# Optimization experiments

Hardware: AMD Instinct MI355X
Metric: run time of the kernel (lower is better)

Reference implementation:

```python
import jax, jax.numpy as jnp
import numpy as np

EPS = 1e-5
NUM_GROUPS = 32
NUM_HEADS = 4


def setup_inputs() -> dict:
    key = jax.random.key(0)
    k1, k2, k3 = jax.random.split(key, 3)
    b, c, h, w = 8, 256, 32, 32
    x = jax.random.normal(k1, (b, c, h, w), dtype=jnp.float32)
    gn_w = jnp.ones((c,), dtype=jnp.float32)
    gn_b = jnp.zeros((c,), dtype=jnp.float32)
    qkv_w = jax.random.normal(k2, (3 * c, c), dtype=jnp.float32) * (1.0 / np.sqrt(c))
    qkv_b = jnp.zeros((3 * c,), dtype=jnp.float32)
    proj_w = jax.random.normal(k3, (c, c), dtype=jnp.float32) * (1.0 / np.sqrt(c))
    proj_b = jnp.zeros((c,), dtype=jnp.float32)
    return {"x": x, "gn_w": gn_w, "gn_b": gn_b, "qkv_w": qkv_w,
            "qkv_b": qkv_b, "proj_w": proj_w, "proj_b": proj_b}


def _group_norm(x, weight, bias):
    # x: (b, c, n)
    b, c, n = x.shape
    xg = x.reshape(b, NUM_GROUPS, (c // NUM_GROUPS) * n)
    mean = jnp.mean(xg, axis=-1, keepdims=True)
    var = jnp.mean(jnp.square(xg - mean), axis=-1, keepdims=True)
    xn = ((xg - mean) * jax.lax.rsqrt(var + EPS)).reshape(b, c, n)
    return xn * weight[None, :, None] + bias[None, :, None]


def reference(x, gn_w, gn_b, qkv_w, qkv_b, proj_w, proj_b):
    b, c, h, w = x.shape
    # FFT2 over spatial dims, then view_as_real -> flatten: seq len N = 2*h*w
    xf = jnp.fft.fft2(x)                                   # (b,c,h,w) complex64
    xr = jnp.stack([xf.real, xf.imag], axis=-1).reshape(b, c, -1)  # (b,c,N)
    n = xr.shape[-1]
    # GroupNorm(32, c) then 1x1 Conv1d producing qkv
    normed = _group_norm(xr, gn_w, gn_b)
    qkv = jnp.einsum('oc,bcn->bon', qkv_w, normed) + qkv_b[None, :, None]  # (b,3c,N)
    # split heads exactly like torch: view(b*H, 3c/H, N) then split along dim 1
    qkv = qkv.reshape(b * NUM_HEADS, 3 * c // NUM_HEADS, n)
    ch = c // NUM_HEADS
    q, k, v = qkv[:, :ch], qkv[:, ch:2 * ch], qkv[:, 2 * ch:]
    scale = ch ** -0.25
    weight = jnp.einsum('bct,bcs->bts', q * scale, k * scale)  # (b*H, N, N)
    weight = jax.nn.softmax(weight, axis=-1)
    a = jnp.einsum('bts,bcs->bct', weight, v).reshape(b, c, n)
    out = jnp.einsum('oc,bcn->bon', proj_w, a) + proj_b[None, :, None]  # (b,c,N)
    # back to complex and IFFT2
    out = out.reshape(b, c, h, w, 2)
    oc = jax.lax.complex(out[..., 0], out[..., 1])
    res = jnp.fft.ifft2(oc)                                # (b,c,h,w) complex64
    # return complex result as real/imag pair
    return jnp.stack([res.real, res.imag], axis=-1)         # (b,c,h,w,2)
```

## Files before the change

kernel.cpp:

```cpp
#include <hip/hip_runtime.h>
#include <hip/hip_bf16.h>

#define PI_F 3.14159265358979323846f
#define C1_EXP 0.18033688f
#define C2_EXP 23.083120f

typedef __bf16 bf16x8 __attribute__((ext_vector_type(8)));
typedef float f32x4 __attribute__((ext_vector_type(4)));
typedef unsigned int uint32x4 __attribute__((ext_vector_type(4)));

__device__ __forceinline__ bf16x8 neg8(bf16x8 v) {
  union { bf16x8 b; uint32x4 u; } x;
  x.b = v;
  x.u ^= (uint32x4){0x80008000u, 0x80008000u, 0x80008000u, 0x80008000u};
  return x.b;
}

#define MFMA3(acc, Ph, Pl, Qh, Ql)                                        \
  acc = __builtin_amdgcn_mfma_f32_16x16x32_bf16(Ph, Qh, acc, 0, 0, 0);    \
  acc = __builtin_amdgcn_mfma_f32_16x16x32_bf16(Ph, Ql, acc, 0, 0, 0);    \
  acc = __builtin_amdgcn_mfma_f32_16x16x32_bf16(Pl, Qh, acc, 0, 0, 0);

__device__ __forceinline__ int slot2n(int slot) {
  const int pi = slot >> 1, im = slot & 1;
  int k1, k2;
  if (pi < 480)      { k1 = 1 + (pi >> 5); k2 = pi & 31; }
  else if (pi < 495) { k1 = 0;  k2 = pi - 479; }
  else if (pi < 510) { k1 = 16; k2 = pi - 494; }
  else if (pi < 514) { k1 = ((pi - 510) >> 1) * 16; k2 = ((pi - 510) & 1) * 16; }
  else               { k1 = 0; k2 = 0; }
  return 2 * (k1 * 32 + k2) + im;
}

__global__ __launch_bounds__(256) void k_twid(__bf16* __restrict__ tw) {
  for (int e = threadIdx.x; e < 1024; e += 256) {
    const int j = e >> 5, k = e & 31;
    const int t = (j * k) & 31;
    float sv, cv;
    sincosf(2.0f * PI_F * (float)t / 32.0f, &sv, &cv);
    const __bf16 ch = (__bf16)cv;
    const __bf16 sh = (__bf16)sv;
    tw[e] = ch;
    tw[1024 + e] = (__bf16)(cv - (float)ch);
    tw[2048 + e] = sh;
    tw[3072 + e] = (__bf16)(sv - (float)sh);
  }
}

__global__ __launch_bounds__(256) void k_fft2(const float* __restrict__ x,
                                              float* __restrict__ xr,
                                              float* __restrict__ stats_raw,
                                              const __bf16* __restrict__ tw) {
  __shared__ __align__(16) char smem[51200];
  const int tid = threadIdx.x, lane = tid & 63, wv = tid >> 6;
  const int quad = lane >> 4, q16 = lane & 15;
  const int slice = blockIdx.x * 4 + wv;
  char* const wr_ = smem + 10240 + wv * 10240;

  const float* xs = x + (size_t)slice * 1024;
  float4 xv[4];
#pragma unroll
  for (int u = 0; u < 4; ++u) xv[u] = ((const float4*)xs)[u * 64 + lane];

  for (int i = tid; i < 512; i += 256) {
    const int t = i >> 7, r = (i >> 2) & 31, c8 = (i & 3) * 8;
    *(uint4*)(smem + t * 2560 + r * 80 + c8 * 2) =
        *(const uint4*)(tw + t * 1024 + r * 32 + c8);
  }

#pragma unroll
  for (int u = 0; u < 4; ++u) {
    const int f = u * 64 + lane;
    const float4 v = xv[u];
    const int row = f >> 3, c4 = (f & 7) * 4;
    union { unsigned long long q; __bf16 b[4]; } ph, pl;
    ph.b[0] = (__bf16)v.x; ph.b[1] = (__bf16)v.y;
    ph.b[2] = (__bf16)v.z; ph.b[3] = (__bf16)v.w;
    pl.b[0] = (__bf16)(v.x - (float)ph.b[0]);
    pl.b[1] = (__bf16)(v.y - (float)ph.b[1]);
    pl.b[2] = (__bf16)(v.z - (float)ph.b[2]);
    pl.b[3] = (__bf16)(v.w - (float)ph.b[3]);
    *(unsigned long long*)(wr_ + row * 80 + c4 * 2) = ph.q;
    *(unsigned long long*)(wr_ + 2560 + row * 80 + c4 * 2) = pl.q;
  }
  __syncthreads();

  bf16x8 cch[2], ccl[2], ssh[2], ssl[2], xh[2], xl[2];
#pragma unroll
  for (int t2 = 0; t2 < 2; ++t2) {
    const int row = t2 * 16 + q16;
    cch[t2] = *(const bf16x8*)(smem + row * 80 + quad * 16);
    ccl[t2] = *(const bf16x8*)(smem + 2560 + row * 80 + quad * 16);
    ssh[t2] = *(const bf16x8*)(smem + 5120 + row * 80 + quad * 16);
    ssl[t2] = *(const bf16x8*)(smem + 7680 + row * 80 + quad * 16);
    xh[t2] = *(const bf16x8*)(wr_ + row * 80 + quad * 16);
    xl[t2] = *(const bf16x8*)(wr_ + 2560 + row * 80 + quad * 16);
  }

  f32x4 yre[2][2] = {}, yim[2][2] = {};
#pragma unroll
  for (int mt = 0; mt < 2; ++mt)
#pragma unroll
    for (int nt = 0; nt < 2; ++nt) {
      MFMA3(yre[mt][nt], xh[mt], xl[mt], cch[nt], ccl[nt]);
      MFMA3(yim[mt][nt], xh[mt], xl[mt], ssh[nt], ssl[nt]);
    }

#pragma unroll
  for (int mt = 0; mt < 2; ++mt)
#pragma unroll
    for (int nt = 0; nt < 2; ++nt) {
      char* base = wr_ + (nt * 16 + q16) * 80 + (mt * 16 + quad * 4) * 2;
      union { unsigned long long q; __bf16 b[4]; } h, l;
#pragma unroll
      for (int r = 0; r < 4; ++r) {
        const float v = yre[mt][nt][r];
        h.b[r] = (__bf16)v; l.b[r] = (__bf16)(v - (float)h.b[r]);
      }
      *(unsigned long long*)(base) = h.q;
      *(unsigned long long*)(base + 2560) = l.q;
#pragma unroll
      for (int r = 0; r < 4; ++r) {
        const float v = -yim[mt][nt][r];
        h.b[r] = (__bf16)v; l.b[r] = (__bf16)(v - (float)h.b[r]);
      }
      *(unsigned long long*)(base + 5120) = h.q;
      *(unsigned long long*)(base + 7680) = l.q;
    }
  asm volatile("" ::: "memory");

  bf16x8 yreh[2], yrel[2], yimh[2], yiml[2];
#pragma unroll
  for (int nt = 0; nt < 2; ++nt) {
    const int row = nt * 16 + q16;
    yreh[nt] = *(const bf16x8*)(wr_ + row * 80 + quad * 16);
    yrel[nt] = *(const bf16x8*)(wr_ + 2560 + row * 80 + quad * 16);
    yimh[nt] = *(const bf16x8*)(wr_ + 5120 + row * 80 + quad * 16);
    yiml[nt] = *(const bf16x8*)(wr_ + 7680 + row * 80 + quad * 16);
  }

  f32x4 zre[2][2] = {}, zim[2][2] = {};
  bf16x8 ssnh[2], ssnl[2];
  ssnh[0] = neg8(ssh[0]); ssnh[1] = neg8(ssh[1]);
  ssnl[0] = neg8(ssl[0]); ssnl[1] = neg8(ssl[1]);
#pragma unroll
  for (int mt = 0; mt < 2; ++mt)
#pragma unroll
    for (int nt = 0; nt < 2; ++nt) {
      MFMA3(zre[mt][nt], cch[mt], ccl[mt], yreh[nt], yrel[nt]);
      MFMA3(zre[mt][nt], ssh[mt], ssl[mt], yimh[nt], yiml[nt]);
      MFMA3(zim[mt][nt], cch[mt], ccl[mt], yimh[nt], yiml[nt]);
      MFMA3(zim[mt][nt], ssnh[mt], ssnl[mt], yreh[nt], yrel[nt]);
    }

  float* op = xr + (size_t)slice * 2048;
  float s1 = 0.f, s2 = 0.f;
#pragma unroll
  for (int mt = 0; mt < 2; ++mt)
#pragma unroll
    for (int nt = 0; nt < 2; ++nt)
#pragma unroll
      for (int r = 0; r < 4; ++r) {
        const int k1 = mt * 16 + quad * 4 + r;
        const int k2 = nt * 16 + q16;
        const float a = zre[mt][nt][r], bimg = zim[mt][nt][r];
        s1 += a + bimg;
        s2 += a * a + bimg * bimg;
        float2 st; st.x = a; st.y = bimg;
        *(float2*)(op + 2 * (k1 * 32 + k2)) = st;
      }
#pragma unroll
  for (int off = 1; off <= 32; off <<= 1) {
    s1 += __shfl_xor(s1, off);
    s2 += __shfl_xor(s2, off);
  }
  if (lane == 0) {
    const int bg = (slice >> 8) * 32 + ((slice & 255) >> 3);
    atomicAdd(&stats_raw[bg * 2], s1);
    atomicAdd(&stats_raw[bg * 2 + 1], s2);
  }
}

__global__ __launch_bounds__(256) void k_uvec(const float* __restrict__ stats_raw,
                                              const float* __restrict__ gn_w,
                                              const float* __restrict__ gn_b,
                                              const float* __restrict__ qkv_w,
                                              const float* __restrict__ qkv_b,
                                              float* __restrict__ uk,
                                              float* __restrict__ uv) {
  const int blk = blockIdx.x;
  const int tid = threadIdx.x;
  const int b = blk >> 3, h = (blk >> 1) & 3, role = blk & 1;
  __shared__ float Bsh[256];
  {
    const int g = tid >> 3;
    const float S = stats_raw[(b * 32 + g) * 2];
    const float S2 = stats_raw[(b * 32 + g) * 2 + 1];
    const float mean = S * (1.0f / 16384.0f);
    const float var = S2 * (1.0f / 16384.0f) - mean * mean;
    const float rstd = rsqrtf(var + 1e-5f);
    Bsh[tid] = gn_b[tid] - mean * rstd * gn_w[tid];
  }
  __syncthreads();
  const int cp = tid >> 2, seg = tid & 3;
  const int row = h * 192 + 64 + role * 64 + cp;
  const float* wr_ = qkv_w + (size_t)row * 256 + seg * 64;
  const float* bs = Bsh + seg * 64;
  float s = 0.f;
#pragma unroll
  for (int i = 0; i < 16; ++i) {
    const float4 w4 = *(const float4*)(wr_ + i * 4);
    const float4 b4 = *(const float4*)(bs + i * 4);
    s += w4.x * b4.x + w4.y * b4.y + w4.z * b4.z + w4.w * b4.w;
  }
  s += __shfl_xor(s, 1);
  s += __shfl_xor(s, 2);
  if (seg == 0) {
    float* dst = (role == 0) ? uk : uv;
    dst[(size_t)(b * 4 + h) * 64 + cp] = s + qkv_b[row];
  }
}

__global__ __launch_bounds__(256) void k_gntrans(const float* __restrict__ xr,
                                                 const float* __restrict__ stats_raw,
                                                 const float* __restrict__ w,
                                                 const float* __restrict__ bias,
                                                 __bf16* __restrict__ xt) {
  const int n0 = blockIdx.x * 64;
  const int c0 = blockIdx.y * 64;
  const int b = blockIdx.z;
  __shared__ __bf16 Lt[64][72];
  const int tid = threadIdx.x;
  for (int i = tid; i < 1024; i += 256) {
    const int cl = i >> 4, c = c0 + cl, nl = (i & 15) * 4;
    const float S = stats_raw[(b * 32 + (c >> 3)) * 2];
    const float S2 = stats_raw[(b * 32 + (c >> 3)) * 2 + 1];
    const float mean = S * (1.0f / 16384.0f);
    const float var = S2 * (1.0f / 16384.0f) - mean * mean;
    const float rstd = rsqrtf(var + 1e-5f);
    const float sc = rstd * w[c];
    const float sh = bias[c] - mean * sc;
    const float4 v = *(const float4*)(xr + ((size_t)b * 256 + c) * 2048 + n0 + nl);
    Lt[nl][cl] = (__bf16)(v.x * sc + sh);
    Lt[nl + 1][cl] = (__bf16)(v.y * sc + sh);
    Lt[nl + 2][cl] = (__bf16)(v.z * sc + sh);
    Lt[nl + 3][cl] = (__bf16)(v.w * sc + sh);
  }
  __syncthreads();
  __bf16* dst = xt + (size_t)b * 524288 + (size_t)n0 * 256 + c0;
  for (int i = tid; i < 512; i += 256) {
    const int nl = i >> 3, cch = (i & 7) * 8;
    *(uint4*)(dst + (size_t)nl * 256 + cch) = *(const uint4*)&Lt[nl][cch];
  }
}

__global__ __launch_bounds__(256) void k_gemm_qkv(const float* __restrict__ W,
                                                  const __bf16* __restrict__ X,
                                                  const float* __restrict__ bias,
                                                  const float* __restrict__ uk,
                                                  float* __restrict__ dq,
                                                  __bf16* __restrict__ Qt,
                                                  __bf16* __restrict__ Kt,
                                                  __bf16* __restrict__ Vt) {
  const int tx = blockIdx.x;
  const int b = blockIdx.y;
  int role, hd, nt;
  if (tx < 64) { role = 0; hd = tx >> 4; nt = tx & 15; }
  else if (tx < 100) { role = 1; const int i = tx - 64; hd = i / 9; nt = i - hd * 9; }
  else { role = 2; const int i = tx - 100; hd = i / 9; nt = i - hd * 9; }
  const int n0 = nt * 128;
  const int bo = hd * 192 + role * 64;
  const __bf16* Xb = X + (size_t)b * 524288;

  __shared__ __align__(16) char smem[30720];
  __bf16 (*Ot)[72] = (__bf16(*)[72])smem;
  __bf16 (*Ot2)[136] = (__bf16(*)[136])smem;

  const int tid = threadIdx.x, lane = tid & 63, wv = tid >> 6;
  const int quad = lane >> 4, q16 = lane & 15, wn = wv * 32;

  const int rowA = tid >> 2, chA = (tid & 3) * 8;
  const int browB0 = tid >> 2, bchB = (tid & 3) * 8;
  const float* wA = W + (size_t)(bo + rowA) * 256 + chA;

  const int s0r = n0 + browB0, s1r = n0 + browB0 + 64;
  const int pn0 = (role == 0) ? s0r : slot2n(s0r);
  const int pn1 = (role == 0) ? s1r : slot2n(s1r);

  float4 aP0 = *(const float4*)(wA);
  float4 aP1 = *(const float4*)(wA + 4);
  uint4 bP0 = *(const uint4*)(Xb + (size_t)pn0 * 256 + bchB);
  uint4 bP1 = *(const uint4*)(Xb + (size_t)pn1 * 256 + bchB);

  f32x4 acc[4][2] = {};
  int bsel = 0;
  for (int k0 = 0; k0 < 256; k0 += 32) {
    char* const Ab = smem + bsel;
    char* const Bb = smem + bsel + 5120;
    {
      union { uint4 u; __bf16 h[8]; } pa;
      pa.h[0] = (__bf16)aP0.x; pa.h[1] = (__bf16)aP0.y;
      pa.h[2] = (__bf16)aP0.z; pa.h[3] = (__bf16)aP0.w;
      pa.h[4] = (__bf16)aP1.x; pa.h[5] = (__bf16)aP1.y;
      pa.h[6] = (__bf16)aP1.z; pa.h[7] = (__bf16)aP1.w;
      *(uint4*)(Ab + rowA * 80 + chA * 2) = pa.u;
      *(uint4*)(Bb + browB0 * 80 + bchB * 2) = bP0;
      *(uint4*)(Bb + (browB0 + 64) * 80 + bchB * 2) = bP1;
    }
    __syncthreads();
    if (k0 + 32 < 256) {
      const int kn = k0 + 32;
      aP0 = *(const float4*)(wA + kn);
      aP1 = *(const float4*)(wA + kn + 4);
      bP0 = *(const uint4*)(Xb + (size_t)pn0 * 256 + kn + bchB);
      bP1 = *(const uint4*)(Xb + (size_t)pn1 * 256 + kn + bchB);
    }
    bf16x8 af[4], bfr[2];
#pragma unroll
    for (int mt = 0; mt < 4; ++mt)
      af[mt] = *(const bf16x8*)(Ab + (mt * 16 + q16) * 80 + quad * 16);
#pragma unroll
    for (int jn = 0; jn < 2; ++jn)
      bfr[jn] = *(const bf16x8*)(Bb + (wn + jn * 16 + q16) * 80 + quad * 16);
#pragma unroll
    for (int mt = 0; mt < 4; ++mt)
#pragma unroll
      for (int jn = 0; jn < 2; ++jn)
        acc[mt][jn] = __builtin_amdgcn_mfma_f32_16x16x32_bf16(af[mt], bfr[jn], acc[mt][jn], 0, 0, 0);
    bsel ^= 15360;
  }
  __syncthreads();

  const int bh = b * 4 + hd;
  if (role == 2) {
#pragma unroll
    for (int mt = 0; mt < 4; ++mt)
#pragma unroll
      for (int r = 0; r < 4; ++r) {
        const int c = mt * 16 + quad * 4 + r;
        const float bv = bias[bo + c];
#pragma unroll
        for (int jn = 0; jn < 2; ++jn)
          Ot2[c][wn + jn * 16 + q16] = (__bf16)(acc[mt][jn][r] + bv);
      }
    __syncthreads();
    __bf16* dst = Vt + (size_t)bh * 73728;
    for (int i = tid; i < 1024; i += 256) {
      const int c = i >> 4, sg = (i & 15) * 8;
      *(uint4*)(dst + (size_t)c * 1152 + n0 + sg) = *(const uint4*)&Ot2[c][sg];
    }
  } else {
    __bf16* dst = (role == 0 ? Qt + (size_t)bh * 131072
                             : Kt + (size_t)bh * 73728);
#pragma unroll
    for (int mt = 0; mt < 4; ++mt)
#pragma unroll
      for (int r = 0; r < 4; ++r) {
        const int c = mt * 16 + quad * 4 + r;
        const float bv = bias[bo + c];
#pragma unroll
        for (int jn = 0; jn < 2; ++jn)
          Ot[wn + jn * 16 + q16][c] = (__bf16)(acc[mt][jn][r] + bv);
      }
    __syncthreads();
    for (int i = tid; i < 1024; i += 256) {
      const int nl = i >> 3, cch = (i & 7) * 8;
      *(uint4*)(dst + (size_t)(n0 + nl) * 64 + cch) = *(const uint4*)&Ot[nl][cch];
    }
    if (role == 0 && tid < 128) {
      const float* ukp = uk + (size_t)bh * 64;
      float dv = 0.f;
#pragma unroll
      for (int g8 = 0; g8 < 8; ++g8) {
        const bf16x8 qv = *(const bf16x8*)&Ot[tid][g8 * 8];
#pragma unroll
        for (int k = 0; k < 8; ++k) dv += (float)qv[k] * ukp[g8 * 8 + k];
      }
      dq[(size_t)bh * 2048 + n0 + tid] = dv * (2.0f * C1_EXP);
    }
  }
}

template <bool EDGE>
__device__ __forceinline__ void attn_iter(
    const int s0, const int send, const int quad,
    const __bf16* __restrict__ kg, const __bf16* __restrict__ vg,
    char* const kw, char* const vw,
    const char* const (&krp)[2][2], const char* const (&vrp)[4],
    char* const (&pwp)[2][2], const char* const (&prp)[2],
    const bf16x8 (&bq)[2][2], const float (&Dm)[2],
    uint4& kA, uint4& vA, f32x4 (&oacc)[2][4],
    float (&lsum)[2], float (&spsum)[2]) {
  *(uint4*)kw = kA;
  *(uint4*)vw = vA;
  __syncthreads();
  if (s0 + 32 < send) {
    kA = *(const uint4*)(kg + (size_t)(s0 + 32) * 64);
    vA = *(const uint4*)(vg + s0 + 32);
  }

  f32x4 sacc[2][2] = {};
#pragma unroll
  for (int j = 0; j < 2; ++j)
#pragma unroll
    for (int kk = 0; kk < 2; ++kk) {
      const bf16x8 ak = *(const bf16x8*)krp[j][kk];
      sacc[0][j] = __builtin_amdgcn_mfma_f32_16x16x32_bf16(ak, bq[0][kk], sacc[0][j], 0, 0, 0);
      sacc[1][j] = __builtin_amdgcn_mfma_f32_16x16x32_bf16(ak, bq[1][kk], sacc[1][j], 0, 0, 0);
    }

#pragma unroll
  for (int b = 0; b < 2; ++b) {
    float lacc = 0.f, spacc = 0.f;
#pragma unroll
    for (int j = 0; j < 2; ++j) {
      float B0, B2, Bv1, Bv3, Bm1, Bm3;
      if (EDGE) {
        const int sg = s0 + j * 16 + quad * 4;
        B0 = (sg < 1020) ? (1.0f - C2_EXP) : ((sg < 1028) ? -C2_EXP : -1e30f);
        B2 = (sg + 2 < 1020) ? (1.0f - C2_EXP)
                             : ((sg + 2 < 1028) ? -C2_EXP : -1e30f);
        Bv1 = (sg + 1 < 1028) ? -C2_EXP : -1e30f;
        Bv3 = (sg + 3 < 1028) ? -C2_EXP : -1e30f;
        Bm1 = (sg + 1 < 1020) ? Dm[b] : -1e30f;
        Bm3 = (sg + 3 < 1020) ? Dm[b] : -1e30f;
      } else {
        B0 = 1.0f - C2_EXP;
        B2 = 1.0f - C2_EXP;
        Bv1 = -C2_EXP;
        Bv3 = -C2_EXP;
        Bm1 = Dm[b];
        Bm3 = Dm[b];
      }
      const float P0  = __builtin_amdgcn_exp2f(fmaf(sacc[b][j][0],  C1_EXP, B0));
      const float Pv1 = __builtin_amdgcn_exp2f(fmaf(sacc[b][j][1],  C1_EXP, Bv1));
      const float P2  = __builtin_amdgcn_exp2f(fmaf(sacc[b][j][2],  C1_EXP, B2));
      const float Pv3 = __builtin_amdgcn_exp2f(fmaf(sacc[b][j][3],  C1_EXP, Bv3));
      const float pm1 = __builtin_amdgcn_exp2f(fmaf(sacc[b][j][1], -C1_EXP, Bm1));
      const float pm3 = __builtin_amdgcn_exp2f(fmaf(sacc[b][j][3], -C1_EXP, Bm3));
      const float mm = pm1 + pm3;
      lacc += (P0 + P2) + (Pv1 + Pv3) + mm;
      spacc += mm;
      union { uint2 u; __bf16 h[4]; } pk;
      pk.h[0] = (__bf16)P0;
      pk.h[1] = (__bf16)(Pv1 - pm1);
      pk.h[2] = (__bf16)P2;
      pk.h[3] = (__bf16)(Pv3 - pm3);
      *(uint2*)pwp[b][j] = pk.u;
    }
    lsum[b] += lacc;
    spsum[b] += spacc;
  }
  asm volatile("" ::: "memory");

  bf16x8 bp[2];
  bp[0] = *(const bf16x8*)prp[0];
  bp[1] = *(const bf16x8*)prp[1];
#pragma unroll
  for (int jc = 0; jc < 4; ++jc) {
    const bf16x8 av = *(const bf16x8*)vrp[jc];
    oacc[0][jc] = __builtin_amdgcn_mfma_f32_16x16x32_bf16(av, bp[0], oacc[0][jc], 0, 0, 0);
    oacc[1][jc] = __builtin_amdgcn_mfma_f32_16x16x32_bf16(av, bp[1], oacc[1][jc], 0, 0, 0);
  }
  __syncthreads();
}

__global__ __launch_bounds__(256, 4) void k_attn_mfma(const __bf16* __restrict__ Qt,
                                                      const __bf16* __restrict__ Kt,
                                                      const __bf16* __restrict__ Vt,
                                                      const float* __restrict__ dq,
                                                      const float* __restrict__ uv,
                                                      __bf16* __restrict__ opart,
                                                      float* __restrict__ lpart) {
  const int t0 = blockIdx.x * 128;
  const int part = blockIdx.y;
  const int bh = blockIdx.z;
  const __bf16* kt = Kt + (size_t)bh * 73728;
  const __bf16* vt = Vt + (size_t)bh * 73728;

  __shared__ __align__(16) char smem[16384];

  const int tid = threadIdx.x, lane = tid & 63, wv = tid >> 6;
  const int quad = lane >> 4, q16 = lane & 15;
  const int wband = wv * 32;

  const int rK = tid >> 3, gK = tid & 7;
  char* const kw = smem + rK * 128 + ((gK ^ (rK & 7)) * 16);
  const int cV = tid >> 2, gV = tid & 3;
  char* const vw = smem + 4096 + (cV >> 1) * 128 +
                   ((((cV & 1) * 4 + gV) ^ ((cV >> 1) & 7)) * 16);
  const __bf16* const kg = kt + (size_t)rK * 64 + gK * 8;
  const __bf16* const vg = vt + (size_t)cV * 1152 + gV * 8;

  const char* krp[2][2];
#pragma unroll
  for (int j = 0; j < 2; ++j)
#pragma unroll
    for (int kk = 0; kk < 2; ++kk)
      krp[j][kk] = smem + (j * 16 + q16) * 128 + (((kk * 4 + quad) ^ (q16 & 7)) * 16);
  const int a7 = (q16 >> 1) & 7, p1 = q16 & 1;
  const char* vrp[4];
#pragma unroll
  for (int jc = 0; jc < 4; ++jc)
    vrp[jc] = smem + 4096 + (jc * 8 + (q16 >> 1)) * 128 +
              (((p1 * 4 + quad) ^ a7) * 16);
  char* pwp[2][2];
  const char* prp[2];
#pragma unroll
  for (int b = 0; b < 2; ++b) {
    const int mrow = ((wband + b * 16) >> 1) + (q16 >> 1);
    prp[b] = smem + 8192 + mrow * 128 + (((p1 * 4 + quad) ^ a7) * 16);
#pragma unroll
    for (int j = 0; j < 2; ++j)
      pwp[b][j] = smem + 8192 + mrow * 128 +
                  (((p1 * 4 + j * 2 + (quad >> 1)) ^ a7) * 16) + (quad & 1) * 8;
  }

  const __bf16* qbase = Qt + (size_t)bh * 131072;
  bf16x8 bq[2][2];
  float Dm[2];
#pragma unroll
  for (int b = 0; b < 2; ++b) {
    const int t = t0 + wband + b * 16 + q16;
    const __bf16* qp = qbase + (size_t)t * 64 + quad * 8;
    bq[b][0] = *(const bf16x8*)qp;
    bq[b][1] = *(const bf16x8*)(qp + 32);
    Dm[b] = dq[(size_t)bh * 2048 + t] - C2_EXP;
  }

  f32x4 oacc[2][4] = {};
  float lsum[2] = {0.f, 0.f};
  float spsum[2] = {0.f, 0.f};

  const int sbase = part * 352, send = sbase + 352;
  const int sInt = (part == 2) ? 992 : send;
  uint4 kA = *(const uint4*)(kg + (size_t)sbase * 64);
  uint4 vA = *(const uint4*)(vg + sbase);

  for (int s0 = sbase; s0 < sInt; s0 += 32)
    attn_iter<false>(s0, send, quad, kg, vg, kw, vw, krp, vrp, pwp, prp,
                     bq, Dm, kA, vA, oacc, lsum, spsum);
  for (int s0 = sInt; s0 < send; s0 += 32)
    attn_iter<true>(s0, send, quad, kg, vg, kw, vw, krp, vrp, pwp, prp,
                    bq, Dm, kA, vA, oacc, lsum, spsum);

  float4 uv4[4];
  {
    const float* uvp = uv + (size_t)bh * 64;
#pragma unroll
    for (int jc = 0; jc < 4; ++jc)
      uv4[jc] = *(const float4*)(uvp + jc * 16 + quad * 4);
  }

#pragma unroll
  for (int b = 0; b < 2; ++b) {
    float l = lsum[b], sp = spsum[b];
    l += __shfl_xor(l, 16);
    l += __shfl_xor(l, 32);
    sp += __shfl_xor(sp, 16);
    sp += __shfl_xor(sp, 32);
    const float sp2 = 2.0f * sp;
    const int t = t0 + wband + b * 16 + q16;
    const size_t row = (size_t)(bh * 3 + part) * 2048 + t;
    if (quad == 0) lpart[row] = l;
    __bf16* opp = opart + row * 64;
#pragma unroll
    for (int jc = 0; jc < 4; ++jc) {
      union { uint2 u; __bf16 h[4]; } pk;
      pk.h[0] = (__bf16)(oacc[b][jc][0] + sp2 * uv4[jc].x);
      pk.h[1] = (__bf16)(oacc[b][jc][1] + sp2 * uv4[jc].y);
      pk.h[2] = (__bf16)(oacc[b][jc][2] + sp2 * uv4[jc].z);
      pk.h[3] = (__bf16)(oacc[b][jc][3] + sp2 * uv4[jc].w);
      *(uint2*)(opp + jc * 16 + quad * 4) = pk.u;
    }
  }
}

__global__ __launch_bounds__(256) void k_gemm_proj(const float* __restrict__ W,
                                                   const __bf16* __restrict__ opart,
                                                   const float* __restrict__ lpart,
                                                   const float* __restrict__ bias,
                                                   float* __restrict__ C) {
  const int n0 = blockIdx.x * 128;
  const int bo = blockIdx.y * 64;
  const int b = blockIdx.z;
  float* Cb = C + (size_t)b * 524288;

  __shared__ __align__(16) char smem[30720];

  const int tid = threadIdx.x, lane = tid & 63, wv = tid >> 6;
  const int quad = lane >> 4, q16 = lane & 15, wn = wv * 32;

  const int rowA = tid >> 2, chA = (tid & 3) * 8;
  const int browB0 = tid >> 2, bchB = (tid & 3) * 8;
  const float* wA = W + (size_t)(bo + rowA) * 256 + chA;

  float linv[2][4];
#pragma unroll
  for (int g = 0; g < 2; ++g) {
    const int t = n0 + browB0 + g * 64;
#pragma unroll
    for (int hd = 0; hd < 4; ++hd) {
      const size_t rr = (size_t)((b * 4 + hd) * 3) * 2048 + t;
      linv[g][hd] = 1.0f / (lpart[rr] + lpart[rr + 2048] + lpart[rr + 4096]);
    }
  }

  float4 aP0 = *(const float4*)(wA);
  float4 aP1 = *(const float4*)(wA + 4);
  bf16x8 oP[2][3];
#pragma unroll
  for (int g = 0; g < 2; ++g) {
    const int t = n0 + browB0 + g * 64;
    const size_t rr = (size_t)(b * 4 * 3) * 2048 + t;
#pragma unroll
    for (int p = 0; p < 3; ++p)
      oP[g][p] = *(const bf16x8*)(opart + (rr + p * 2048) * 64 + bchB);
  }

  f32x4 acc[4][2] = {};
  int bsel = 0;
  for (int k0 = 0; k0 < 256; k0 += 32) {
    char* const Ab = smem + bsel;
    char* const Bb = smem + bsel + 5120;
    {
      union { uint4 u; __bf16 h[8]; } pa;
      pa.h[0] = (__bf16)aP0.x; pa.h[1] = (__bf16)aP0.y;
      pa.h[2] = (__bf16)aP0.z; pa.h[3] = (__bf16)aP0.w;
      pa.h[4] = (__bf16)aP1.x; pa.h[5] = (__bf16)aP1.y;
      pa.h[6] = (__bf16)aP1.z; pa.h[7] = (__bf16)aP1.w;
      *(uint4*)(Ab + rowA * 80 + chA * 2) = pa.u;
      const int hd = (k0 + bchB) >> 6;
#pragma unroll
      for (int g = 0; g < 2; ++g) {
        const float inv = linv[g][hd];
        bf16x8 res;
#pragma unroll
        for (int k = 0; k < 8; ++k)
          res[k] = (__bf16)((((float)oP[g][0][k] + (float)oP[g][1][k]) +
                             (float)oP[g][2][k]) * inv);
        *(bf16x8*)(Bb + (browB0 + g * 64) * 80 + bchB * 2) = res;
      }
    }
    __syncthreads();
    if (k0 + 32 < 256) {
      const int kn = k0 + 32;
      aP0 = *(const float4*)(wA + kn);
      aP1 = *(const float4*)(wA + kn + 4);
      const int c = kn + bchB;
      const int hd = c >> 6, cu = c & 63;
#pragma unroll
      for (int g = 0; g < 2; ++g) {
        const int t = n0 + browB0 + g * 64;
        const size_t rr = (size_t)((b * 4 + hd) * 3) * 2048 + t;
#pragma unroll
        for (int p = 0; p < 3; ++p)
          oP[g][p] = *(const bf16x8*)(opart + (rr + p * 2048) * 64 + cu);
      }
    }
    bf16x8 af[4], bfr[2];
#pragma unroll
    for (int mt = 0; mt < 4; ++mt)
      af[mt] = *(const bf16x8*)(Ab + (mt * 16 + q16) * 80 + quad * 16);
#pragma unroll
    for (int jn = 0; jn < 2; ++jn)
      bfr[jn] = *(const bf16x8*)(Bb + (wn + jn * 16 + q16) * 80 + quad * 16);
#pragma unroll
    for (int mt = 0; mt < 4; ++mt)
#pragma unroll
      for (int jn = 0; jn < 2; ++jn)
        acc[mt][jn] = __builtin_amdgcn_mfma_f32_16x16x32_bf16(af[mt], bfr[jn], acc[mt][jn], 0, 0, 0);
    bsel ^= 15360;
  }

#pragma unroll
  for (int mt = 0; mt < 4; ++mt)
#pragma unroll
    for (int r = 0; r < 4; ++r) {
      const int o = bo + mt * 16 + quad * 4 + r;
      const float bv = bias[o];
#pragma unroll
      for (int jn = 0; jn < 2; ++jn)
        Cb[(size_t)o * 2048 + n0 + wn + jn * 16 + q16] = acc[mt][jn][r] + bv;
    }
}

__global__ __launch_bounds__(256) void k_ifft2(const float* __restrict__ spec,
                                               float* __restrict__ out,
                                               const __bf16* __restrict__ tw) {
  __shared__ __align__(16) char smem[51200];
  const int tid = threadIdx.x, lane = tid & 63, wv = tid >> 6;
  const int quad = lane >> 4, q16 = lane & 15;
  const int slice = blockIdx.x * 4 + wv;
  char* const wr_ = smem + 10240 + wv * 10240;

  const float* sp = spec + (size_t)slice * 2048;
  float4 sv8[8];
#pragma unroll
  for (int u = 0; u < 8; ++u) sv8[u] = ((const float4*)sp)[u * 64 + lane];

  for (int i = tid; i < 512; i += 256) {
    const int t = i >> 7, r = (i >> 2) & 31, c8 = (i & 3) * 8;
    *(uint4*)(smem + t * 2560 + r * 80 + c8 * 2) =
        *(const uint4*)(tw + t * 1024 + r * 32 + c8);
  }

#pragma unroll
  for (int u = 0; u < 8; ++u) {
    const int f = u * 64 + lane;
    const float4 v = sv8[u];
    const int k1 = f >> 4, k2 = (f & 15) * 2;
    char* base = wr_ + k1 * 80 + k2 * 2;
    union { unsigned int w; __bf16 b[2]; } p;
    const __bf16 rh0 = (__bf16)v.x, rh1 = (__bf16)v.z;
    const __bf16 ih0 = (__bf16)v.y, ih1 = (__bf16)v.w;
    p.b[0] = rh0; p.b[1] = rh1; *(unsigned int*)(base) = p.w;
    p.b[0] = (__bf16)(v.x - (float)rh0);
    p.b[1] = (__bf16)(v.z - (float)rh1); *(unsigned int*)(base + 2560) = p.w;
    p.b[0] = ih0; p.b[1] = ih1; *(unsigned int*)(base + 5120) = p.w;
    p.b[0] = (__bf16)(v.y - (float)ih0);
    p.b[1] = (__bf16)(v.w - (float)ih1); *(unsigned int*)(base + 7680) = p.w;
  }
  __syncthreads();

  bf16x8 cch[2], ccl[2], ssh[2], ssl[2], ssnh[2], ssnl[2];
  bf16x8 xreh[2], xrel[2], ximh[2], ximl[2];
#pragma unroll
  for (int t2 = 0; t2 < 2; ++t2) {
    const int row = t2 * 16 + q16;
    cch[t2] = *(const bf16x8*)(smem + row * 80 + quad * 16);
    ccl[t2] = *(const bf16x8*)(smem + 2560 + row * 80 + quad * 16);
    ssh[t2] = *(const bf16x8*)(smem + 5120 + row * 80 + quad * 16);
    ssl[t2] = *(const bf16x8*)(smem + 7680 + row * 80 + quad * 16);
    xreh[t2] = *(const bf16x8*)(wr_ + row * 80 + quad * 16);
    xrel[t2] = *(const bf16x8*)(wr_ + 2560 + row * 80 + quad * 16);
    ximh[t2] = *(const bf16x8*)(wr_ + 5120 + row * 80 + quad * 16);
    ximl[t2] = *(const bf16x8*)(wr_ + 7680 + row * 80 + quad * 16);
  }
  ssnh[0] = neg8(ssh[0]); ssnh[1] = neg8(ssh[1]);
  ssnl[0] = neg8(ssl[0]); ssnl[1] = neg8(ssl[1]);

  f32x4 yre[2][2] = {}, yim[2][2] = {};
#pragma unroll
  for (int mt = 0; mt < 2; ++mt)
#pragma unroll
    for (int nt = 0; nt < 2; ++nt) {
      MFMA3(yre[mt][nt], xreh[mt], xrel[mt], cch[nt], ccl[nt]);
      MFMA3(yre[mt][nt], ximh[mt], ximl[mt], ssnh[nt], ssnl[nt]);
      MFMA3(yim[mt][nt], xreh[mt], xrel[mt], ssh[nt], ssl[nt]);
      MFMA3(yim[mt][nt], ximh[mt], ximl[mt], cch[nt], ccl[nt]);
    }

#pragma unroll
  for (int mt = 0; mt < 2; ++mt)
#pragma unroll
    for (int nt = 0; nt < 2; ++nt) {
      char* base = wr_ + (nt * 16 + q16) * 80 + (mt * 16 + quad * 4) * 2;
      union { unsigned long long q; __bf16 b[4]; } h, l;
#pragma unroll
      for (int r = 0; r < 4; ++r) {
        const float v = yre[mt][nt][r];
        h.b[r] = (__bf16)v; l.b[r] = (__bf16)(v - (float)h.b[r]);
      }
      *(unsigned long long*)(base) = h.q;
      *(unsigned long long*)(base + 2560) = l.q;
#pragma unroll
      for (int r = 0; r < 4; ++r) {
        const float v = yim[mt][nt][r];
        h.b[r] = (__bf16)v; l.b[r] = (__bf16)(v - (float)h.b[r]);
      }
      *(unsigned long long*)(base + 5120) = h.q;
      *(unsigned long long*)(base + 7680) = l.q;
    }
  asm volatile("" ::: "memory");

  bf16x8 yreh[2], yrel[2], yimh[2], yiml[2];
#pragma unroll
  for (int nt = 0; nt < 2; ++nt) {
    const int row = nt * 16 + q16;
    yreh[nt] = *(const bf16x8*)(wr_ + row * 80 + quad * 16);
    yrel[nt] = *(const bf16x8*)(wr_ + 2560 + row * 80 + quad * 16);
    yimh[nt] = *(const bf16x8*)(wr_ + 5120 + row * 80 + quad * 16);
    yiml[nt] = *(const bf16x8*)(wr_ + 7680 + row * 80 + quad * 16);
  }

  f32x4 zre[2][2] = {}, zim[2][2] = {};
#pragma unroll
  for (int mt = 0; mt < 2; ++mt)
#pragma unroll
    for (int nt = 0; nt < 2; ++nt) {
      MFMA3(zre[mt][nt], cch[mt], ccl[mt], yreh[nt], yrel[nt]);
      MFMA3(zre[mt][nt], ssnh[mt], ssnl[mt], yimh[nt], yiml[nt]);
      MFMA3(zim[mt][nt], cch[mt], ccl[mt], yimh[nt], yiml[nt]);
      MFMA3(zim[mt][nt], ssh[mt], ssl[mt], yreh[nt], yrel[nt]);
    }

  float* op = out + (size_t)slice * 2048;
#pragma unroll
  for (int mt = 0; mt < 2; ++mt)
#pragma unroll
    for (int nt = 0; nt < 2; ++nt)
#pragma unroll
      for (int r = 0; r < 4; ++r) {
        const int n1 = mt * 16 + quad * 4 + r;
        const int n2 = nt * 16 + q16;
        float2 st;
        st.x = zre[mt][nt][r] * (1.0f / 1024.0f);
        st.y = zim[mt][nt][r] * (1.0f / 1024.0f);
        *(float2*)(op + 2 * (n1 * 32 + n2)) = st;
      }
}

extern "C" void kernel_launch(void* const* d_in, const int* in_sizes, int n_in,
                              void* d_out, int out_size, void* d_ws, size_t ws_size,
                              hipStream_t stream) {
  (void)in_sizes; (void)n_in; (void)out_size; (void)ws_size;
  const float* x      = (const float*)d_in[0];
  const float* gn_w   = (const float*)d_in[1];
  const float* gn_b   = (const float*)d_in[2];
  const float* qkv_w  = (const float*)d_in[3];
  const float* qkv_b  = (const float*)d_in[4];
  const float* proj_w = (const float*)d_in[5];
  const float* proj_b = (const float*)d_in[6];
  float* out = (float*)d_out;

  float* spec  = (float*)d_ws;
  __bf16* Qt   = (__bf16*)(spec + 4194304);
  __bf16* Kt   = Qt + 4194304;
  __bf16* Vt   = Kt + 2359296;
  float* stats = (float*)(Vt + 2359296);
  float* xr    = stats + 512;
  __bf16* xt   = (__bf16*)(xr + 4194304);
  __bf16* opart = (__bf16*)xr;
  float*  lpart = (float*)(opart + 12582912);
  float*  dq    = lpart + 196608;
  float*  uk    = dq + 65536;
  float*  uv    = uk + 2048;
  __bf16* tw    = (__bf16*)(uv + 2048);

  hipMemsetAsync(stats, 0, 512 * sizeof(float), stream);
  k_twid<<<1, 256, 0, stream>>>(tw);
  k_fft2<<<512, 256, 0, stream>>>(x, xr, stats, tw);
  k_uvec<<<64, 256, 0, stream>>>(stats, gn_w, gn_b, qkv_w, qkv_b, uk, uv);
  k_gntrans<<<dim3(32, 4, 8), 256, 0, stream>>>(xr, stats, gn_w, gn_b, xt);
  k_gemm_qkv<<<dim3(136, 8), 256, 0, stream>>>(qkv_w, xt, qkv_b, uk, dq,
                                               Qt, Kt, Vt);
  k_attn_mfma<<<dim3(16, 3, 32), 256, 0, stream>>>(Qt, Kt, Vt, dq, uv,
                                                   opart, lpart);
  k_gemm_proj<<<dim3(16, 4, 8), 256, 0, stream>>>(proj_w, opart, lpart,
                                                  proj_b, spec);
  k_ifft2<<<512, 256, 0, stream>>>(spec, out, tw);
}
```

Measured before the change: 169.6 us.

## Double-buffer K/V tiles in LDS and raise wave priority around MFMA blocks

```diff
diff --git a/kernel.cpp b/kernel.cpp
--- a/kernel.cpp
+++ b/kernel.cpp
@@ -1,5 +1,6 @@
 #include <hip/hip_runtime.h>
 #include <hip/hip_bf16.h>
+#include <stdint.h>
 
 #define PI_F 3.14159265358979323846f
 #define C1_EXP 0.18033688f
@@ -385,21 +386,14 @@
 __device__ __forceinline__ void attn_iter(
     const int s0, const int send, const int quad,
     const __bf16* __restrict__ kg, const __bf16* __restrict__ vg,
-    char* const kw, char* const vw,
-    const char* const (&krp)[2][2], const char* const (&vrp)[4],
+    char*& kw, char*& vw,
+    const char* (&krp)[2][2], const char* (&vrp)[4],
     char* const (&pwp)[2][2], const char* const (&prp)[2],
     const bf16x8 (&bq)[2][2], const float (&Dm)[2],
     uint4& kA, uint4& vA, f32x4 (&oacc)[2][4],
     float (&lsum)[2], float (&spsum)[2]) {
-  *(uint4*)kw = kA;
-  *(uint4*)vw = vA;
-  __syncthreads();
-  if (s0 + 32 < send) {
-    kA = *(const uint4*)(kg + (size_t)(s0 + 32) * 64);
-    vA = *(const uint4*)(vg + s0 + 32);
-  }
-
   f32x4 sacc[2][2] = {};
+  __builtin_amdgcn_s_setprio(1);
 #pragma unroll
   for (int j = 0; j < 2; ++j)
 #pragma unroll
@@ -408,6 +402,16 @@
       sacc[0][j] = __builtin_amdgcn_mfma_f32_16x16x32_bf16(ak, bq[0][kk], sacc[0][j], 0, 0, 0);
       sacc[1][j] = __builtin_amdgcn_mfma_f32_16x16x32_bf16(ak, bq[1][kk], sacc[1][j], 0, 0, 0);
     }
+  __builtin_amdgcn_s_setprio(0);
+
+  if (s0 + 32 < send) {
+    *(uint4*)kw = kA;
+    *(uint4*)vw = vA;
+  }
+  if (s0 + 64 < send) {
+    kA = *(const uint4*)(kg + (size_t)(s0 + 64) * 64);
+    vA = *(const uint4*)(vg + s0 + 64);
+  }
 
 #pragma unroll
   for (int b = 0; b < 2; ++b) {
@@ -456,13 +460,26 @@
   bf16x8 bp[2];
   bp[0] = *(const bf16x8*)prp[0];
   bp[1] = *(const bf16x8*)prp[1];
+  __builtin_amdgcn_s_setprio(1);
 #pragma unroll
   for (int jc = 0; jc < 4; ++jc) {
     const bf16x8 av = *(const bf16x8*)vrp[jc];
     oacc[0][jc] = __builtin_amdgcn_mfma_f32_16x16x32_bf16(av, bp[0], oacc[0][jc], 0, 0, 0);
     oacc[1][jc] = __builtin_amdgcn_mfma_f32_16x16x32_bf16(av, bp[1], oacc[1][jc], 0, 0, 0);
   }
+  __builtin_amdgcn_s_setprio(0);
   __syncthreads();
+
+  kw = (char*)((uintptr_t)kw ^ 4096);
+  vw = (char*)((uintptr_t)vw ^ 4096);
+#pragma unroll
+  for (int j = 0; j < 2; ++j)
+#pragma unroll
+    for (int kk = 0; kk < 2; ++kk)
+      krp[j][kk] = (const char*)((uintptr_t)krp[j][kk] ^ 4096);
+#pragma unroll
+  for (int jc = 0; jc < 4; ++jc)
+    vrp[jc] = (const char*)((uintptr_t)vrp[jc] ^ 4096);
 }
 
 __global__ __launch_bounds__(256, 4) void k_attn_mfma(const __bf16* __restrict__ Qt,
@@ -478,17 +495,17 @@
   const __bf16* kt = Kt + (size_t)bh * 73728;
   const __bf16* vt = Vt + (size_t)bh * 73728;
 
-  __shared__ __align__(16) char smem[16384];
+  __shared__ __align__(16) char smem[24576];
 
   const int tid = threadIdx.x, lane = tid & 63, wv = tid >> 6;
   const int quad = lane >> 4, q16 = lane & 15;
   const int wband = wv * 32;
 
   const int rK = tid >> 3, gK = tid & 7;
-  char* const kw = smem + rK * 128 + ((gK ^ (rK & 7)) * 16);
+  char* kw = smem + rK * 128 + ((gK ^ (rK & 7)) * 16);
   const int cV = tid >> 2, gV = tid & 3;
-  char* const vw = smem + 4096 + (cV >> 1) * 128 +
-                   ((((cV & 1) * 4 + gV) ^ ((cV >> 1) & 7)) * 16);
+  char* vw = smem + 8192 + (cV >> 1) * 128 +
+             ((((cV & 1) * 4 + gV) ^ ((cV >> 1) & 7)) * 16);
   const __bf16* const kg = kt + (size_t)rK * 64 + gK * 8;
   const __bf16* const vg = vt + (size_t)cV * 1152 + gV * 8;
 
@@ -502,17 +519,17 @@
   const char* vrp[4];
 #pragma unroll
   for (int jc = 0; jc < 4; ++jc)
-    vrp[jc] = smem + 4096 + (jc * 8 + (q16 >> 1)) * 128 +
+    vrp[jc] = smem + 8192 + (jc * 8 + (q16 >> 1)) * 128 +
               (((p1 * 4 + quad) ^ a7) * 16);
   char* pwp[2][2];
   const char* prp[2];
 #pragma unroll
   for (int b = 0; b < 2; ++b) {
     const int mrow = ((wband + b * 16) >> 1) + (q16 >> 1);
-    prp[b] = smem + 8192 + mrow * 128 + (((p1 * 4 + quad) ^ a7) * 16);
+    prp[b] = smem + 16384 + mrow * 128 + (((p1 * 4 + quad) ^ a7) * 16);
 #pragma unroll
     for (int j = 0; j < 2; ++j)
-      pwp[b][j] = smem + 8192 + mrow * 128 +
+      pwp[b][j] = smem + 16384 + mrow * 128 +
                   (((p1 * 4 + j * 2 + (quad >> 1)) ^ a7) * 16) + (quad & 1) * 8;
   }
 
@@ -534,8 +551,16 @@
 
   const int sbase = part * 352, send = sbase + 352;
   const int sInt = (part == 2) ? 992 : send;
+
   uint4 kA = *(const uint4*)(kg + (size_t)sbase * 64);
   uint4 vA = *(const uint4*)(vg + sbase);
+  *(uint4*)kw = kA;
+  *(uint4*)vw = vA;
+  kA = *(const uint4*)(kg + (size_t)(sbase + 32) * 64);
+  vA = *(const uint4*)(vg + sbase + 32);
+  __syncthreads();
+  kw = (char*)((uintptr_t)kw ^ 4096);
+  vw = (char*)((uintptr_t)vw ^ 4096);
 
   for (int s0 = sbase; s0 < sInt; s0 += 32)
     attn_iter<false>(s0, send, quad, kg, vg, kw, vw, krp, vrp, pwp, prp,
```

Measured after the change: 180.5 us. 1.06x slower.
